# Performance work log

Measured on AMD Instinct MI355X. Metric: run time of the kernel, lower is better.

Reference implementation:

```python
import jax, jax.numpy as jnp
import numpy as np

B, T, D, H = 64, 512, 512, 1024


def setup_inputs() -> dict:
    key = jax.random.key(0)
    k1, k2, k3 = jax.random.split(key, 3)
    x = jax.random.normal(k1, (B, T, D), dtype=jnp.float32)
    W = jax.random.normal(k2, (D, 4 * H), dtype=jnp.float32) * 0.02  # input kernel
    U = jax.random.normal(k3, (H, 4 * H), dtype=jnp.float32) * 0.02  # recurrent kernel
    b = jnp.zeros((4 * H,), dtype=jnp.float32)
    return {"x": x, "W": W, "U": U, "b": b}


def reference(x, W, U, b):
    # Keras LSTM, gate order [i, f, c(g), o], sigmoid recurrent activation, tanh activation.
    # return_sequences=False, return_state=True -> pred == h_T; output = concat([h_T, h_T, c_T]).
    batch = x.shape[0]
    hidden = U.shape[0]

    def step(carry, xt):
        h, c = carry
        z = xt @ W + h @ U + b  # [B, 4H]
        i, f, g, o = jnp.split(z, 4, axis=-1)
        i = jax.nn.sigmoid(i)
        f = jax.nn.sigmoid(f)
        o = jax.nn.sigmoid(o)
        c_new = f * c + i * jnp.tanh(g)
        h_new = o * jnp.tanh(c_new)
        return (h_new, c_new), None

    h0 = jnp.zeros((batch, hidden), dtype=x.dtype)
    c0 = jnp.zeros((batch, hidden), dtype=x.dtype)
    xs = jnp.swapaxes(x, 0, 1)  # [T, B, D]
    (hT, cT), _ = jax.lax.scan(step, (h0, c0), xs)
    return jnp.concatenate([hT, hT, cT], axis=-1)  # [B, 3H]
```

## Files before the change

kernel.cpp:

```cpp
#include <hip/hip_runtime.h>
#include <stdint.h>

typedef unsigned short u16;

#define T_STEPS 512
#define BATCH   64
#define DIN     512
#define HID     1024
#define G4      4096
#define NBLK    128
#define NH      8
#define NC      32
#define THREADS 512

#define U_LD    1032
#define W_LD    520

#define SM_BYTES 99328
#define WT_OFF   66048
#define HS_OFF   33792

typedef float f32x16 __attribute__((ext_vector_type(16)));
typedef short bf16x8 __attribute__((ext_vector_type(8)));
typedef unsigned uint32x4 __attribute__((ext_vector_type(4)));

__device__ __forceinline__ u16 f2bf(float f) {
  unsigned u = __float_as_uint(f);
  u += 0x7fffu + ((u >> 16) & 1u);
  return (u16)(u >> 16);
}
__device__ __forceinline__ float sigm(float x) {
  return __builtin_amdgcn_rcpf(1.f + __expf(-x));
}
__device__ __forceinline__ float fast_tanh(float x) {
  return 1.f - 2.f * __builtin_amdgcn_rcpf(__expf(2.f * x) + 1.f);
}

__device__ __forceinline__ uint32x4 load16_sc(uint64_t addr) {
  uint32x4 d;
  asm volatile("global_load_dwordx4 %0, %1, off sc0 sc1" : "=v"(d) : "v"(addr));
  return d;
}
__device__ __forceinline__ unsigned load4_sc(uint64_t addr) {
  unsigned d;
  asm volatile("global_load_dword %0, %1, off sc0 sc1" : "=v"(d) : "v"(addr));
  return d;
}
__device__ __forceinline__ void store16_sc(uint64_t addr, uint32x4 v) {
  asm volatile("global_store_dwordx4 %0, %1, off sc0 sc1" :: "v"(addr), "v"(v) : "memory");
}
__device__ __forceinline__ void store4_sc(uint64_t addr, unsigned v) {
  asm volatile("global_store_dword %0, %1, off sc0 sc1" :: "v"(addr), "v"(v) : "memory");
}
#define WAITV(n) asm volatile("s_waitcnt vmcnt(" #n ")" ::: "memory")

__global__ void cvt_x(const float* __restrict__ x, u16* __restrict__ xb) {
  int i = blockIdx.x * 256 + threadIdx.x;
  int dblk = i & 63;
  int rest = i >> 6;
  int b = rest & 63;
  int t = rest >> 6;
  const float4* s = reinterpret_cast<const float4*>(x + ((size_t)(b * T_STEPS + t)) * DIN + dblk * 8);
  float4 f0 = s[0], f1 = s[1];
  uint4 o;
  o.x = (unsigned)f2bf(f0.x) | ((unsigned)f2bf(f0.y) << 16);
  o.y = (unsigned)f2bf(f0.z) | ((unsigned)f2bf(f0.w) << 16);
  o.z = (unsigned)f2bf(f1.x) | ((unsigned)f2bf(f1.y) << 16);
  o.w = (unsigned)f2bf(f1.z) | ((unsigned)f2bf(f1.w) << 16);
  *reinterpret_cast<uint4*>(xb + ((size_t)(t * BATCH + b)) * DIN + dblk * 8) = o;
}

__launch_bounds__(THREADS)
__global__ void lstm_kernel(const float* __restrict__ W, const float* __restrict__ U,
                            const float* __restrict__ bias, const u16* __restrict__ xb,
                            u16* __restrict__ hbuf, float* __restrict__ out,
                            unsigned* __restrict__ flags) {
  __shared__ __align__(16) char smraw[SM_BYTES];
  u16* Ut = (u16*)smraw;
  u16* Wt = (u16*)(smraw + WT_OFF);
  float* zp = (float*)smraw;
  u16* hstage = (u16*)(smraw + HS_OFF);

  const int tid = threadIdx.x;
  const int bid = blockIdx.x;
  const int j0 = bid * NH;

  for (int idx = tid; idx < NC * HID; idx += THREADS) {
    int c = idx & (NC - 1);
    int k = idx >> 5;
    int gcol = ((c >> 3) << 10) + j0 + (c & 7);
    Ut[c * U_LD + k] = f2bf(U[(size_t)k * G4 + gcol]);
  }
  for (int idx = tid; idx < NC * DIN; idx += THREADS) {
    int c = idx & (NC - 1);
    int k = idx >> 5;
    int gcol = ((c >> 3) << 10) + j0 + (c & 7);
    Wt[c * W_LD + k] = f2bf(W[(size_t)k * G4 + gcol]);
  }
  __syncthreads();

  const int l   = tid & 63;
  const int wv  = tid >> 6;
  const int m_t = wv & 1;
  const int ks  = wv >> 1;
  const int cl  = l & 31;
  const int q   = l >> 5;

  bf16x8 ubf[16], wbf[8];
  {
    const u16* ub = Ut + cl * U_LD + ks * 256 + q * 8;
#pragma unroll
    for (int s = 0; s < 16; ++s) ubf[s] = *(const bf16x8*)(ub + s * 16);
    const u16* wb = Wt + cl * W_LD + ks * 128 + q * 8;
#pragma unroll
    for (int s = 0; s < 8; ++s) wbf[s] = *(const bf16x8*)(wb + s * 16);
  }
  __syncthreads();

  const int row = m_t * 32 + cl;
  const int pb = tid & 63;
  const int pu = tid >> 6;
  float c_reg = 0.f;
  const float bi  = bias[j0 + pu];
  const float bf_ = bias[1024 + j0 + pu];
  const float bg  = bias[2048 + j0 + pu];
  const float bo  = bias[3072 + j0 + pu];

  const uint64_t fbase = (uint64_t)flags;
  const uint64_t faddr = fbase + (uint64_t)(ks * 32 + cl) * 16;
  const uint64_t hlane = (uint64_t)(ks * 32 + q) * 1024 + (uint64_t)row * 16;

#define HMFMA(S) acc = __builtin_amdgcn_mfma_f32_32x32x16_bf16( \
    __builtin_bit_cast(bf16x8, abuf[S]), ubf[S], acc, 0, 0, 0)

  for (int t = 0; t < T_STEPS; ++t) {
    f32x16 acc = {0.f,0.f,0.f,0.f,0.f,0.f,0.f,0.f,0.f,0.f,0.f,0.f,0.f,0.f,0.f,0.f};

    const u16* xa = xb + (size_t)t * (BATCH * DIN) + row * DIN + ks * 128 + q * 8;
#pragma unroll
    for (int s = 0; s < 8; ++s) {
      bf16x8 av = *(const bf16x8*)(xa + s * 16);
      acc = __builtin_amdgcn_mfma_f32_32x32x16_bf16(av, wbf[s], acc, 0, 0, 0);
    }

    while (true) {
      unsigned f = load4_sc(faddr);
      WAITV(0);
      if (__all(f >= (unsigned)t)) break;
      __builtin_amdgcn_s_sleep(1);
    }

    const uint64_t hb = (uint64_t)hbuf + (uint64_t)(t & 1) * (BATCH * HID * 2) + hlane;
    uint32x4 abuf[16];
#pragma unroll
    for (int s = 0; s < 16; ++s) abuf[s] = load16_sc(hb + (uint64_t)s * 2048);
    WAITV(12); __builtin_amdgcn_sched_barrier(0);
    HMFMA(0); HMFMA(1); HMFMA(2); HMFMA(3);
    WAITV(8); __builtin_amdgcn_sched_barrier(0);
    HMFMA(4); HMFMA(5); HMFMA(6); HMFMA(7);
    WAITV(4); __builtin_amdgcn_sched_barrier(0);
    HMFMA(8); HMFMA(9); HMFMA(10); HMFMA(11);
    WAITV(0); __builtin_amdgcn_sched_barrier(0);
    HMFMA(12); HMFMA(13); HMFMA(14); HMFMA(15);

#pragma unroll
    for (int r = 0; r < 16; ++r) {
      int rl = (r & 3) + 8 * (r >> 2) + 4 * q;
      zp[ks * 2112 + (m_t * 32 + rl) * 33 + cl] = acc[r];
    }
    __syncthreads();

    float zi = bi, zf = bf_, zg = bg, zo = bo;
#pragma unroll
    for (int k2 = 0; k2 < 4; ++k2) {
      const float* zr = zp + k2 * 2112 + pb * 33;
      zi += zr[pu]; zf += zr[pu + 8]; zg += zr[pu + 16]; zo += zr[pu + 24];
    }
    float ig = sigm(zi), fg = sigm(zf), og = sigm(zo);
    float gg = fast_tanh(zg);
    c_reg = fg * c_reg + ig * gg;
    float h = og * fast_tanh(c_reg);
    hstage[pb * 8 + pu] = f2bf(h);
    if (t == T_STEPS - 1) {
      float* orow = out + (size_t)pb * 3072 + j0 + pu;
      orow[0]    = h;
      orow[1024] = h;
      orow[2048] = c_reg;
    }
    __syncthreads();

    if (wv == 0) {
      uint32x4 hv = *reinterpret_cast<const uint32x4*>(&hstage[l * 8]);
      uint64_t hbn = (uint64_t)hbuf + (uint64_t)((t + 1) & 1) * (BATCH * HID * 2);
      store16_sc(hbn + (uint64_t)bid * 1024 + (uint64_t)l * 16, hv);
      WAITV(0);
      if (l == 0) store4_sc(fbase + (uint64_t)bid * 16, (unsigned)(t + 1));
    }
  }
#undef HMFMA
}

extern "C" void kernel_launch(void* const* d_in, const int* in_sizes, int n_in,
                              void* d_out, int out_size, void* d_ws, size_t ws_size,
                              hipStream_t stream) {
  const float* x = (const float*)d_in[0];
  const float* W = (const float*)d_in[1];
  const float* U = (const float*)d_in[2];
  const float* b = (const float*)d_in[3];
  float* out = (float*)d_out;

  const size_t xb_bytes   = (size_t)T_STEPS * BATCH * DIN * sizeof(u16);
  const size_t hbuf_bytes = 2ull * BATCH * HID * sizeof(u16);
  const size_t flag_bytes = NBLK * 16;
  if (ws_size < xb_bytes + hbuf_bytes + flag_bytes) return;

  u16* xb         = (u16*)d_ws;
  u16* hbuf       = (u16*)((char*)d_ws + xb_bytes);
  unsigned* flags = (unsigned*)((char*)d_ws + xb_bytes + hbuf_bytes);

  hipMemsetAsync((void*)hbuf, 0, hbuf_bytes + flag_bytes, stream);
  cvt_x<<<(T_STEPS * BATCH * DIN / 8 + 255) / 256, 256, 0, stream>>>(x, xb);
  lstm_kernel<<<NBLK, THREADS, 0, stream>>>(W, U, b, xb, hbuf, out, flags);
}
```

Before: 2.656 ms.

## Split batch into two independent groups with 16 hidden units per block

Repartitions the persistent LSTM grid so each block handles 32 batch rows and 16 hidden units, in two batch groups of 64 blocks. Each group has its own h buffer and flags, so a block waits on only 64 producers instead of 128, and each block fetches half as much h per step. Each block now computes 64 gate columns; the weights are staged in two phases through a smaller shared buffer, and the gate reduction reads a float4 from a padded layout. Each block still holds the same number of weights in registers but does less h traffic, and spin-waiting contention is shared across two independent groups.

Result: slower. 2.778 ms (+4.6%).

```diff
diff --git a/kernel.cpp b/kernel.cpp
--- a/kernel.cpp
+++ b/kernel.cpp
@@ -8,17 +8,23 @@
 #define DIN     512
 #define HID     1024
 #define G4      4096
-#define NBLK    128
-#define NH      8
-#define NC      32
 #define THREADS 512
+#define GRPS    2
+#define NBG     64
+#define UPB     16
 
 #define U_LD    1032
 #define W_LD    520
 
-#define SM_BYTES 99328
-#define WT_OFF   66048
-#define HS_OFF   33792
+#define SM_BYTES 66048
+#define HS_OFF   35328
+
+#define XB_BYTES ((size_t)T_STEPS * BATCH * DIN * 2)
+#define HB_OFF   XB_BYTES
+#define HB_GRP   (2u * 32 * HID * 2)
+#define FLG_OFF  (HB_OFF + (size_t)GRPS * HB_GRP)
+#define FLG_GRP  1024
+#define WS_NEED  (FLG_OFF + (size_t)GRPS * FLG_GRP)
 
 typedef float f32x16 __attribute__((ext_vector_type(16)));
 typedef short bf16x8 __attribute__((ext_vector_type(8)));
@@ -72,63 +78,73 @@
 
 __launch_bounds__(THREADS)
 __global__ void lstm_kernel(const float* __restrict__ W, const float* __restrict__ U,
-                            const float* __restrict__ bias, const u16* __restrict__ xb,
-                            u16* __restrict__ hbuf, float* __restrict__ out,
-                            unsigned* __restrict__ flags) {
-  __shared__ __align__(16) char smraw[SM_BYTES];
-  u16* Ut = (u16*)smraw;
-  u16* Wt = (u16*)(smraw + WT_OFF);
-  float* zp = (float*)smraw;
-  u16* hstage = (u16*)(smraw + HS_OFF);
+                            const float* __restrict__ bias, char* __restrict__ ws,
+                            float* __restrict__ out) {
+  __shared__ __align__(16) char sm[SM_BYTES];
+  u16* stage  = (u16*)sm;
+  float* zp   = (float*)sm;
+  u16* hstage = (u16*)(sm + HS_OFF);
 
   const int tid = threadIdx.x;
   const int bid = blockIdx.x;
-  const int j0 = bid * NH;
-
-  for (int idx = tid; idx < NC * HID; idx += THREADS) {
-    int c = idx & (NC - 1);
-    int k = idx >> 5;
-    int gcol = ((c >> 3) << 10) + j0 + (c & 7);
-    Ut[c * U_LD + k] = f2bf(U[(size_t)k * G4 + gcol]);
+  const int nb  = bid & 63;
+  const int grp = bid >> 6;
+
+  const int l    = tid & 63;
+  const int wv   = tid >> 6;
+  const int n_t  = wv & 1;
+  const int ks   = wv >> 1;
+  const int cl   = l & 31;
+  const int q    = l >> 5;
+
+  bf16x8 ubf[16], wbf[8];
+#pragma unroll
+  for (int ph = 0; ph < 2; ++ph) {
+    for (int idx = tid; idx < 32 * HID; idx += THREADS) {
+      int cc = idx & 31, k = idx >> 5;
+      int c = ph * 32 + cc;
+      int gcol = ((c & 3) << 10) + nb * UPB + (c >> 2);
+      stage[cc * U_LD + k] = f2bf(U[(size_t)k * G4 + gcol]);
+    }
+    __syncthreads();
+    if (n_t == ph) {
+      const u16* ub = stage + cl * U_LD + ks * 256 + q * 8;
+#pragma unroll
+      for (int s = 0; s < 16; ++s) ubf[s] = *(const bf16x8*)(ub + s * 16);
+    }
+    __syncthreads();
   }
-  for (int idx = tid; idx < NC * DIN; idx += THREADS) {
-    int c = idx & (NC - 1);
-    int k = idx >> 5;
-    int gcol = ((c >> 3) << 10) + j0 + (c & 7);
-    Wt[c * W_LD + k] = f2bf(W[(size_t)k * G4 + gcol]);
+#pragma unroll
+  for (int ph = 0; ph < 2; ++ph) {
+    for (int idx = tid; idx < 32 * DIN; idx += THREADS) {
+      int cc = idx & 31, k = idx >> 5;
+      int c = ph * 32 + cc;
+      int gcol = ((c & 3) << 10) + nb * UPB + (c >> 2);
+      stage[cc * W_LD + k] = f2bf(W[(size_t)k * G4 + gcol]);
+    }
+    __syncthreads();
+    if (n_t == ph) {
+      const u16* wb = stage + cl * W_LD + ks * 128 + q * 8;
+#pragma unroll
+      for (int s = 0; s < 8; ++s) wbf[s] = *(const bf16x8*)(wb + s * 16);
+    }
+    __syncthreads();
   }
-  __syncthreads();
-
-  const int l   = tid & 63;
-  const int wv  = tid >> 6;
-  const int m_t = wv & 1;
-  const int ks  = wv >> 1;
-  const int cl  = l & 31;
-  const int q   = l >> 5;
-
-  bf16x8 ubf[16], wbf[8];
-  {
-    const u16* ub = Ut + cl * U_LD + ks * 256 + q * 8;
-#pragma unroll
-    for (int s = 0; s < 16; ++s) ubf[s] = *(const bf16x8*)(ub + s * 16);
-    const u16* wb = Wt + cl * W_LD + ks * 128 + q * 8;
-#pragma unroll
-    for (int s = 0; s < 8; ++s) wbf[s] = *(const bf16x8*)(wb + s * 16);
-  }
-  __syncthreads();
-
-  const int row = m_t * 32 + cl;
-  const int pb = tid & 63;
-  const int pu = tid >> 6;
+
+  const int pb = tid & 31;
+  const int pu = tid >> 5;
+  const int j  = nb * UPB + pu;
   float c_reg = 0.f;
-  const float bi  = bias[j0 + pu];
-  const float bf_ = bias[1024 + j0 + pu];
-  const float bg  = bias[2048 + j0 + pu];
-  const float bo  = bias[3072 + j0 + pu];
-
-  const uint64_t fbase = (uint64_t)flags;
-  const uint64_t faddr = fbase + (uint64_t)(ks * 32 + cl) * 16;
-  const uint64_t hlane = (uint64_t)(ks * 32 + q) * 1024 + (uint64_t)row * 16;
+  const float bi  = bias[j];
+  const float bf_ = bias[1024 + j];
+  const float bg  = bias[2048 + j];
+  const float bo  = bias[3072 + j];
+
+  const u16* xb = (const u16*)ws;
+  const uint64_t hgrp = (uint64_t)ws + HB_OFF + (uint64_t)grp * HB_GRP;
+  const uint64_t fgrp = (uint64_t)ws + FLG_OFF + (uint64_t)grp * FLG_GRP;
+  const uint64_t faddr = fgrp + (uint64_t)(ks * 16 + (l & 15)) * 16;
+  const uint64_t hlane = (uint64_t)(ks * 32 + q) * 512 + (uint64_t)cl * 16;
 
 #define HMFMA(S) acc = __builtin_amdgcn_mfma_f32_32x32x16_bf16( \
     __builtin_bit_cast(bf16x8, abuf[S]), ubf[S], acc, 0, 0, 0)
@@ -136,11 +152,11 @@
   for (int t = 0; t < T_STEPS; ++t) {
     f32x16 acc = {0.f,0.f,0.f,0.f,0.f,0.f,0.f,0.f,0.f,0.f,0.f,0.f,0.f,0.f,0.f,0.f};
 
-    const u16* xa = xb + (size_t)t * (BATCH * DIN) + row * DIN + ks * 128 + q * 8;
+    const u16* xa = xb + ((size_t)t * BATCH + grp * 32 + cl) * DIN + ks * 128 + q * 8;
 #pragma unroll
     for (int s = 0; s < 8; ++s) {
-      bf16x8 av = *(const bf16x8*)(xa + s * 16);
-      acc = __builtin_amdgcn_mfma_f32_32x32x16_bf16(av, wbf[s], acc, 0, 0, 0);
+      bf16x8 xv = *(const bf16x8*)(xa + s * 16);
+      acc = __builtin_amdgcn_mfma_f32_32x32x16_bf16(xv, wbf[s], acc, 0, 0, 0);
     }
 
     while (true) {
@@ -150,10 +166,10 @@
       __builtin_amdgcn_s_sleep(1);
     }
 
-    const uint64_t hb = (uint64_t)hbuf + (uint64_t)(t & 1) * (BATCH * HID * 2) + hlane;
+    const uint64_t hb = hgrp + (uint64_t)(t & 1) * 65536 + hlane;
     uint32x4 abuf[16];
 #pragma unroll
-    for (int s = 0; s < 16; ++s) abuf[s] = load16_sc(hb + (uint64_t)s * 2048);
+    for (int s = 0; s < 16; ++s) abuf[s] = load16_sc(hb + (uint64_t)s * 1024);
     WAITV(12); __builtin_amdgcn_sched_barrier(0);
     HMFMA(0); HMFMA(1); HMFMA(2); HMFMA(3);
     WAITV(8); __builtin_amdgcn_sched_barrier(0);
@@ -166,23 +182,23 @@
 #pragma unroll
     for (int r = 0; r < 16; ++r) {
       int rl = (r & 3) + 8 * (r >> 2) + 4 * q;
-      zp[ks * 2112 + (m_t * 32 + rl) * 33 + cl] = acc[r];
+      zp[ks * 2208 + rl * 69 + n_t * 32 + cl] = acc[r];
     }
     __syncthreads();
 
     float zi = bi, zf = bf_, zg = bg, zo = bo;
 #pragma unroll
     for (int k2 = 0; k2 < 4; ++k2) {
-      const float* zr = zp + k2 * 2112 + pb * 33;
-      zi += zr[pu]; zf += zr[pu + 8]; zg += zr[pu + 16]; zo += zr[pu + 24];
+      float4 zv = *(const float4*)(zp + k2 * 2208 + pb * 69 + pu * 4);
+      zi += zv.x; zf += zv.y; zg += zv.z; zo += zv.w;
     }
     float ig = sigm(zi), fg = sigm(zf), og = sigm(zo);
     float gg = fast_tanh(zg);
     c_reg = fg * c_reg + ig * gg;
     float h = og * fast_tanh(c_reg);
-    hstage[pb * 8 + pu] = f2bf(h);
+    hstage[(pu >> 3) * 256 + pb * 8 + (pu & 7)] = f2bf(h);
     if (t == T_STEPS - 1) {
-      float* orow = out + (size_t)pb * 3072 + j0 + pu;
+      float* orow = out + (size_t)(grp * 32 + pb) * 3072 + j;
       orow[0]    = h;
       orow[1024] = h;
       orow[2048] = c_reg;
@@ -190,11 +206,12 @@
     __syncthreads();
 
     if (wv == 0) {
-      uint32x4 hv = *reinterpret_cast<const uint32x4*>(&hstage[l * 8]);
-      uint64_t hbn = (uint64_t)hbuf + (uint64_t)((t + 1) & 1) * (BATCH * HID * 2);
-      store16_sc(hbn + (uint64_t)bid * 1024 + (uint64_t)l * 16, hv);
+      uint32x4 hv = *(const uint32x4*)(hstage + l * 8);
+      uint64_t dst = hgrp + (uint64_t)((t + 1) & 1) * 65536 +
+                     (uint64_t)nb * 1024 + (uint64_t)l * 16;
+      store16_sc(dst, hv);
       WAITV(0);
-      if (l == 0) store4_sc(fbase + (uint64_t)bid * 16, (unsigned)(t + 1));
+      if (l == 0) store4_sc(fgrp + (uint64_t)nb * 16, (unsigned)(t + 1));
     }
   }
 #undef HMFMA
@@ -209,16 +226,10 @@
   const float* b = (const float*)d_in[3];
   float* out = (float*)d_out;
 
-  const size_t xb_bytes   = (size_t)T_STEPS * BATCH * DIN * sizeof(u16);
-  const size_t hbuf_bytes = 2ull * BATCH * HID * sizeof(u16);
-  const size_t flag_bytes = NBLK * 16;
-  if (ws_size < xb_bytes + hbuf_bytes + flag_bytes) return;
-
-  u16* xb         = (u16*)d_ws;
-  u16* hbuf       = (u16*)((char*)d_ws + xb_bytes);
-  unsigned* flags = (unsigned*)((char*)d_ws + xb_bytes + hbuf_bytes);
-
-  hipMemsetAsync((void*)hbuf, 0, hbuf_bytes + flag_bytes, stream);
+  if (ws_size < WS_NEED) return;
+
+  u16* xb = (u16*)d_ws;
+  hipMemsetAsync((char*)d_ws + HB_OFF, 0, WS_NEED - HB_OFF, stream);
   cvt_x<<<(T_STEPS * BATCH * DIN / 8 + 255) / 256, 256, 0, stream>>>(x, xb);
-  lstm_kernel<<<NBLK, THREADS, 0, stream>>>(W, U, b, xb, hbuf, out, flags);
-}
+  lstm_kernel<<<GRPS * NBG, THREADS, 0, stream>>>(W, U, b, (char*)d_ws, out);
+}
```
